# Optimization experiments

Hardware: AMD Instinct MI355X
Metric: run time of the kernel (lower is better)

## Reference

```python
import jax, jax.numpy as jnp
import numpy as np

N_HEAD, D_K = 8, 16

def _ln(x, g, b):
    m = jnp.mean(x, -1, keepdims=True)
    v = jnp.var(x, -1, keepdims=True)
    return (x - m) * jax.lax.rsqrt(v + 1e-5) * g + b

def _enc_layer(x, wq, bq, wk, bk, wv, bv, wo, bo, g1, be1, cw1, cb1, cw2, cb2, g2, be2):
    B, L, D = x.shape
    q = (x @ wq + bq).reshape(B, L, N_HEAD, D_K)
    k = (x @ wk + bk).reshape(B, L, N_HEAD, D_K)
    v = (x @ wv + bv).reshape(B, L, N_HEAD, D_K)
    attn = jnp.einsum('blhd,bmhd->bhlm', q, k) / jnp.sqrt(jnp.float32(D_K))
    attn = jax.nn.softmax(attn, axis=-1)
    o = jnp.einsum('bhlm,bmhd->blhd', attn, v).reshape(B, L, -1)
    x = _ln(o @ wo + bo + x, g1, be1)          # post-LN residual (MHA)
    h = jax.nn.relu(x @ cw1 + cb1)             # 1x1 conv == linear
    return _ln(h @ cw2 + cb2 + x, g2, be2)     # post-LN residual (FFN)

def setup_inputs() -> dict:
    key = jax.random.key(0)
    ks = jax.random.split(key, 20)
    N, D, NNZ = 100000, 128, 2000000
    B, L, NL, DI = 32, 256, 2, 512
    s = 0.02
    inp = {}
    inp['ego'] = jax.random.normal(ks[0], (N, D), jnp.float32)
    inp['vals'] = jax.random.uniform(ks[1], (NNZ,), jnp.float32) / 20.0  # ~normalized adj values
    inp['W1'] = jax.random.normal(ks[2], (D, D), jnp.float32) * s
    inp['b1'] = jnp.zeros((D,), jnp.float32)
    inp['W2'] = jax.random.normal(ks[3], (D, D), jnp.float32) * s
    inp['b2'] = jnp.zeros((D,), jnp.float32)
    inp['enc_in'] = jax.random.normal(ks[4], (B, L, D), jnp.float32)
    inp['wq'] = jax.random.normal(ks[5], (NL, D, D), jnp.float32) * s
    inp['bq'] = jnp.zeros((NL, D), jnp.float32)
    inp['wk'] = jax.random.normal(ks[6], (NL, D, D), jnp.float32) * s
    inp['bk'] = jnp.zeros((NL, D), jnp.float32)
    inp['wv'] = jax.random.normal(ks[7], (NL, D, D), jnp.float32) * s
    inp['bv'] = jnp.zeros((NL, D), jnp.float32)
    inp['wo'] = jax.random.normal(ks[8], (NL, D, D), jnp.float32) * s
    inp['bo'] = jnp.zeros((NL, D), jnp.float32)
    inp['ln1_g'] = jnp.ones((NL, D), jnp.float32)
    inp['ln1_b'] = jnp.zeros((NL, D), jnp.float32)
    inp['cw1'] = jax.random.normal(ks[9], (NL, D, DI), jnp.float32) * s
    inp['cb1'] = jnp.zeros((NL, DI), jnp.float32)
    inp['cw2'] = jax.random.normal(ks[10], (NL, DI, D), jnp.float32) * s
    inp['cb2'] = jnp.zeros((NL, D), jnp.float32)
    inp['ln2_g'] = jnp.ones((NL, D), jnp.float32)
    inp['ln2_b'] = jnp.zeros((NL, D), jnp.float32)
    inp['rows'] = jnp.sort(jax.random.randint(ks[11], (NNZ,), 0, N, jnp.int32))
    inp['cols'] = jax.random.randint(ks[12], (NNZ,), 0, N, jnp.int32)
    return inp

def reference(ego, vals, W1, b1, W2, b2, enc_in, wq, bq, wk, bk, wv, bv, wo, bo,
              ln1_g, ln1_b, cw1, cb1, cw2, cb2, ln2_g, ln2_b, rows, cols):
    N = ego.shape[0]
    # sparse A_in @ ego  (COO SpMM via gather + segment_sum)
    side = jax.ops.segment_sum(vals[:, None] * ego[cols], rows, num_segments=N)
    # bi-interaction aggregator (dropout=identity in eval)
    sum_emb = jax.nn.leaky_relu((ego + side) @ W1 + b1)
    bi_emb = jax.nn.leaky_relu((ego * side) @ W2 + b2)
    agg = sum_emb + bi_emb
    # transformer encoder over edge sequences
    x = enc_in
    for i in range(wq.shape[0]):
        x = _enc_layer(x, wq[i], bq[i], wk[i], bk[i], wv[i], bv[i], wo[i], bo[i],
                       ln1_g[i], ln1_b[i], cw1[i], cb1[i], cw2[i], cb2[i], ln2_g[i], ln2_b[i])
    return (agg, x)
```

## Files before the change

### kernel.cpp

```cpp
#include <hip/hip_runtime.h>

typedef __attribute__((ext_vector_type(8))) short bf16x8;
typedef __attribute__((ext_vector_type(4))) float f32x4;

__device__ __forceinline__ unsigned short f2b(float f) {
    union { float f; unsigned int i; } u; u.f = f;
    return (unsigned short)((u.i + 0x7FFFu + ((u.i >> 16) & 1u)) >> 16);
}
__device__ __forceinline__ unsigned int packbf2(float a, float b) {
    return (unsigned int)f2b(a) | ((unsigned int)f2b(b) << 16);
}

__device__ __forceinline__ void spmm_block(
    const unsigned int* __restrict__ egob, const float* __restrict__ vals,
    const int* __restrict__ rows, const int* __restrict__ cols,
    float* __restrict__ side, int nnz, int blk)
{
    int tid = threadIdx.x;
    int wave = tid >> 6, lane = tid & 63;
    int e0 = blk * 256 + wave * 64;
    if (e0 >= nnz) return;

    int idx = e0 + lane;
    int last = nnz - 1;
    bool ok = idx < nnz;
    int safe = ok ? idx : last;
    int my_row = rows[safe];
    int my_col = cols[safe];
    float my_val = ok ? vals[safe] : 0.f;

    unsigned int pre[16];
    #pragma unroll
    for (int j = 0; j < 16; ++j) {
        unsigned int c = (unsigned int)__builtin_amdgcn_readlane(my_col, j);
        pre[j] = *(egob + ((size_t)c << 6) + lane);
    }

    float ax = 0.f, ay = 0.f;
    int cur = __builtin_amdgcn_readlane(my_row, 0);
    #pragma unroll
    for (int e = 0; e < 64; ++e) {
        int r = __builtin_amdgcn_readlane(my_row, e);
        float vv = __int_as_float(__builtin_amdgcn_readlane(__float_as_int(my_val), e));
        unsigned int u = pre[e & 15];
        if (e < 48) {
            unsigned int c = (unsigned int)__builtin_amdgcn_readlane(my_col, e + 16);
            pre[e & 15] = *(egob + ((size_t)c << 6) + lane);
        }
        if (r != cur) {
            atomicAdd(&side[(size_t)cur * 128 + lane * 2], ax);
            atomicAdd(&side[(size_t)cur * 128 + lane * 2 + 1], ay);
            ax = 0.f; ay = 0.f; cur = r;
        }
        ax = fmaf(vv, __uint_as_float(u << 16), ax);
        ay = fmaf(vv, __uint_as_float(u & 0xFFFF0000u), ay);
    }
    atomicAdd(&side[(size_t)cur * 128 + lane * 2], ax);
    atomicAdd(&side[(size_t)cur * 128 + lane * 2 + 1], ay);
}

#define LDAB 40
#define LDBI2 136
#define LDKV 16

__device__ __forceinline__ void gemm2_core(
    const float* __restrict__ A, const float* __restrict__ W,
    const float* __restrict__ bias, const float* __restrict__ R,
    const float* __restrict__ g, const float* __restrict__ bta,
    float* __restrict__ C, int M, int N, int K, int act,
    int bm, int bn, unsigned short* As, unsigned short* Bs,
    float* redS, float* redSS)
{
    int tid = threadIdx.x, wave = tid >> 6, lane = tid & 63;
    int lm = lane & 15, quad = lane >> 4;
    int wm = wave >> 1, wn = wave & 1;

    f32x4 acc[2][4];
    #pragma unroll
    for (int i = 0; i < 2; ++i)
        #pragma unroll
        for (int j = 0; j < 4; ++j) acc[i][j] = (f32x4)(0.f);

    for (int k0 = 0; k0 < K; k0 += 32) {
        {
            int m = tid >> 2, kc = (tid & 3) * 8;
            const float* p = A + (size_t)(bm + m) * K + k0 + kc;
            float4 a0 = *(const float4*)p, a1 = *(const float4*)(p + 4);
            uint4 pk;
            pk.x = packbf2(a0.x, a0.y); pk.y = packbf2(a0.z, a0.w);
            pk.z = packbf2(a1.x, a1.y); pk.w = packbf2(a1.z, a1.w);
            *(uint4*)&As[m * LDAB + kc] = pk;
        }
        {
            int nn = tid & 127, kh = (tid >> 7) * 16;
            const float* p = W + (size_t)(k0 + kh) * N + bn + nn;
            float w[16];
            #pragma unroll
            for (int j = 0; j < 16; ++j) w[j] = p[(size_t)j * N];
            uint4 pk;
            pk.x = packbf2(w[0], w[1]);  pk.y = packbf2(w[2], w[3]);
            pk.z = packbf2(w[4], w[5]);  pk.w = packbf2(w[6], w[7]);
            *(uint4*)&Bs[nn * LDAB + kh] = pk;
            pk.x = packbf2(w[8], w[9]);  pk.y = packbf2(w[10], w[11]);
            pk.z = packbf2(w[12], w[13]); pk.w = packbf2(w[14], w[15]);
            *(uint4*)&Bs[nn * LDAB + kh + 8] = pk;
        }
        __syncthreads();
        bf16x8 af[2], bfr[4];
        #pragma unroll
        for (int mi = 0; mi < 2; ++mi)
            af[mi] = *(bf16x8*)&As[(wm * 32 + mi * 16 + lm) * LDAB + quad * 8];
        #pragma unroll
        for (int ni = 0; ni < 4; ++ni)
            bfr[ni] = *(bf16x8*)&Bs[(wn * 64 + ni * 16 + lm) * LDAB + quad * 8];
        #pragma unroll
        for (int mi = 0; mi < 2; ++mi)
            #pragma unroll
            for (int ni = 0; ni < 4; ++ni)
                acc[mi][ni] = __builtin_amdgcn_mfma_f32_16x16x32_bf16(
                    af[mi], bfr[ni], acc[mi][ni], 0, 0, 0);
        __syncthreads();
    }

    #pragma unroll
    for (int mi = 0; mi < 2; ++mi) {
        #pragma unroll
        for (int r = 0; r < 4; ++r) {
            int row = bm + wm * 32 + mi * 16 + quad * 4 + r;
            #pragma unroll
            for (int ni = 0; ni < 4; ++ni) {
                int col = bn + wn * 64 + ni * 16 + lm;
                float v = acc[mi][ni][r] + bias[col];
                if (R) v += R[(size_t)row * N + col];
                if (act) v = fmaxf(v, 0.f);
                acc[mi][ni][r] = v;
            }
        }
    }

    if (g) {
        #pragma unroll
        for (int mi = 0; mi < 2; ++mi) {
            #pragma unroll
            for (int r = 0; r < 4; ++r) {
                float s = 0.f, ss = 0.f;
                #pragma unroll
                for (int ni = 0; ni < 4; ++ni) {
                    float v = acc[mi][ni][r];
                    s += v; ss = fmaf(v, v, ss);
                }
                #pragma unroll
                for (int off = 1; off < 16; off <<= 1) {
                    s  += __shfl_xor(s, off, 64);
                    ss += __shfl_xor(ss, off, 64);
                }
                if (lm == 0) {
                    int lr = wm * 32 + mi * 16 + quad * 4 + r;
                    redS[wn * 64 + lr] = s;
                    redSS[wn * 64 + lr] = ss;
                }
            }
        }
        __syncthreads();
        #pragma unroll
        for (int mi = 0; mi < 2; ++mi) {
            #pragma unroll
            for (int r = 0; r < 4; ++r) {
                int lr = wm * 32 + mi * 16 + quad * 4 + r;
                int row = bm + lr;
                float s = redS[lr] + redS[64 + lr];
                float ss = redSS[lr] + redSS[64 + lr];
                float mean = s * (1.f / 128.f);
                float var = ss * (1.f / 128.f) - mean * mean;
                float rstd = rsqrtf(var + 1e-5f);
                #pragma unroll
                for (int ni = 0; ni < 4; ++ni) {
                    int col = wn * 64 + ni * 16 + lm;
                    float y = (acc[mi][ni][r] - mean) * rstd * g[col] + bta[col];
                    C[(size_t)row * 128 + col] = y;
                }
            }
        }
    } else {
        #pragma unroll
        for (int mi = 0; mi < 2; ++mi) {
            #pragma unroll
            for (int r = 0; r < 4; ++r) {
                int row = bm + wm * 32 + mi * 16 + quad * 4 + r;
                #pragma unroll
                for (int ni = 0; ni < 4; ++ni) {
                    int col = bn + wn * 64 + ni * 16 + lm;
                    C[(size_t)row * N + col] = acc[mi][ni][r];
                }
            }
        }
    }
}

__device__ __forceinline__ void bi_core4(
    const float* __restrict__ ego, const float* __restrict__ side,
    const unsigned short* __restrict__ W1t, const unsigned short* __restrict__ W2t,
    const float* __restrict__ b1, const float* __restrict__ b2,
    float* __restrict__ out, int M, int bm,
    unsigned short* Us, unsigned short* Ms)
{
    int tid = threadIdx.x, wave = tid >> 6, lane = tid & 63;
    int lm = lane & 15, quad = lane >> 4;
    int wm = wave >> 1, wn = wave & 1;

    f32x4 acc1[2][4], acc2[2][4];
    #pragma unroll
    for (int i = 0; i < 2; ++i)
        #pragma unroll
        for (int j = 0; j < 4; ++j) { acc1[i][j] = (f32x4)(0.f); acc2[i][j] = (f32x4)(0.f); }

    {
        int m = tid >> 2, kc = (tid & 3) * 32;
        int gm = bm + m;
        float e[32], s[32];
        if (gm < M) {
            const float* pe = ego + (size_t)gm * 128 + kc;
            const float* ps = side + (size_t)gm * 128 + kc;
            #pragma unroll
            for (int j = 0; j < 8; ++j) {
                float4 ev = *(const float4*)(pe + j * 4);
                float4 sv = *(const float4*)(ps + j * 4);
                e[j*4+0] = ev.x; e[j*4+1] = ev.y; e[j*4+2] = ev.z; e[j*4+3] = ev.w;
                s[j*4+0] = sv.x; s[j*4+1] = sv.y; s[j*4+2] = sv.z; s[j*4+3] = sv.w;
            }
        } else {
            #pragma unroll
            for (int j = 0; j < 32; ++j) { e[j] = 0.f; s[j] = 0.f; }
        }
        #pragma unroll
        for (int j = 0; j < 4; ++j) {
            int b0 = j * 8;
            uint4 pu, pv;
            pu.x = packbf2(e[b0+0]+s[b0+0], e[b0+1]+s[b0+1]);
            pu.y = packbf2(e[b0+2]+s[b0+2], e[b0+3]+s[b0+3]);
            pu.z = packbf2(e[b0+4]+s[b0+4], e[b0+5]+s[b0+5]);
            pu.w = packbf2(e[b0+6]+s[b0+6], e[b0+7]+s[b0+7]);
            pv.x = packbf2(e[b0+0]*s[b0+0], e[b0+1]*s[b0+1]);
            pv.y = packbf2(e[b0+2]*s[b0+2], e[b0+3]*s[b0+3]);
            pv.z = packbf2(e[b0+4]*s[b0+4], e[b0+5]*s[b0+5]);
            pv.w = packbf2(e[b0+6]*s[b0+6], e[b0+7]*s[b0+7]);
            *(uint4*)&Us[m * LDBI2 + kc + b0] = pu;
            *(uint4*)&Ms[m * LDBI2 + kc + b0] = pv;
        }
    }
    __syncthreads();

    #pragma unroll
    for (int ks = 0; ks < 4; ++ks) {
        bf16x8 au[2], am[2], bf1[4], bf2[4];
        #pragma unroll
        for (int mi = 0; mi < 2; ++mi) {
            int off = (wm * 32 + mi * 16 + lm) * LDBI2 + ks * 32 + quad * 8;
            au[mi] = *(bf16x8*)&Us[off];
            am[mi] = *(bf16x8*)&Ms[off];
        }
        #pragma unroll
        for (int ni = 0; ni < 4; ++ni) {
            size_t n = (size_t)(wn * 64 + ni * 16 + lm);
            size_t koff = n * 128 + ks * 32 + quad * 8;
            bf1[ni] = *(const bf16x8*)(W1t + koff);
            bf2[ni] = *(const bf16x8*)(W2t + koff);
        }
        #pragma unroll
        for (int mi = 0; mi < 2; ++mi)
            #pragma unroll
            for (int ni = 0; ni < 4; ++ni) {
                acc1[mi][ni] = __builtin_amdgcn_mfma_f32_16x16x32_bf16(
                    au[mi], bf1[ni], acc1[mi][ni], 0, 0, 0);
                acc2[mi][ni] = __builtin_amdgcn_mfma_f32_16x16x32_bf16(
                    am[mi], bf2[ni], acc2[mi][ni], 0, 0, 0);
            }
    }
    #pragma unroll
    for (int mi = 0; mi < 2; ++mi) {
        #pragma unroll
        for (int r = 0; r < 4; ++r) {
            int row = bm + wm * 32 + mi * 16 + quad * 4 + r;
            if (row < M) {
                #pragma unroll
                for (int ni = 0; ni < 4; ++ni) {
                    int col = wn * 64 + ni * 16 + lm;
                    float v1 = acc1[mi][ni][r] + b1[col];
                    v1 = v1 > 0.f ? v1 : 0.01f * v1;
                    float v2 = acc2[mi][ni][r] + b2[col];
                    v2 = v2 > 0.f ? v2 : 0.01f * v2;
                    out[(size_t)row * 128 + col] = v1 + v2;
                }
            }
        }
    }
}

__device__ __forceinline__ void attn_block(
    const float* __restrict__ q, const float* __restrict__ k,
    const float* __restrict__ v, float* __restrict__ o, int NH,
    int blk, float* Ks, float* Vs)
{
    const int L = 256, DK = 16;
    int bh = blk >> 2, qq = blk & 3;
    int b = bh / NH, h = bh % NH;
    int tid = threadIdx.x;
    int qi = tid >> 2, seg = tid & 3;

    int lq = qq * 64 + qi;
    size_t qbase = ((size_t)(b * L + lq) * NH + h) * DK;
    float qr[16];
    #pragma unroll
    for (int d4 = 0; d4 < 4; ++d4) {
        float4 t = *(const float4*)(q + qbase + d4 * 4);
        qr[d4*4+0] = t.x * 0.25f; qr[d4*4+1] = t.y * 0.25f;
        qr[d4*4+2] = t.z * 0.25f; qr[d4*4+3] = t.w * 0.25f;
    }
    float acc[16];
    #pragma unroll
    for (int d = 0; d < 16; ++d) acc[d] = 0.f;
    float mmax = -1e30f, ssum = 0.f;

    for (int c0 = 0; c0 < L; c0 += 128) {
        __syncthreads();
        for (int i = tid; i < 128 * 4; i += 256) {
            int ll = i >> 2, d4 = (i & 3) * 4;
            size_t gg = ((size_t)(b * L + c0 + ll) * NH + h) * DK + d4;
            *(float4*)&Ks[ll * LDKV + d4] = *(const float4*)(k + gg);
            *(float4*)&Vs[ll * LDKV + d4] = *(const float4*)(v + gg);
        }
        __syncthreads();

        for (int i = 0; i < 32; ++i) {
            int kk = (i << 2) | seg;
            const float* kr = &Ks[kk * LDKV];
            float dot = 0.f;
            #pragma unroll
            for (int d4 = 0; d4 < 4; ++d4) {
                float4 kv = *(const float4*)&kr[d4 * 4];
                dot = fmaf(qr[d4*4+0], kv.x, dot);
                dot = fmaf(qr[d4*4+1], kv.y, dot);
                dot = fmaf(qr[d4*4+2], kv.z, dot);
                dot = fmaf(qr[d4*4+3], kv.w, dot);
            }
            if (dot > mmax) {
                float alpha = __expf(mmax - dot);
                ssum *= alpha;
                #pragma unroll
                for (int d = 0; d < 16; ++d) acc[d] *= alpha;
                mmax = dot;
            }
            float p = __expf(dot - mmax);
            ssum += p;
            const float* vr = &Vs[kk * LDKV];
            #pragma unroll
            for (int d4 = 0; d4 < 4; ++d4) {
                float4 vv = *(const float4*)&vr[d4 * 4];
                acc[d4*4+0] = fmaf(p, vv.x, acc[d4*4+0]);
                acc[d4*4+1] = fmaf(p, vv.y, acc[d4*4+1]);
                acc[d4*4+2] = fmaf(p, vv.z, acc[d4*4+2]);
                acc[d4*4+3] = fmaf(p, vv.w, acc[d4*4+3]);
            }
        }
    }

    float m1 = fmaxf(mmax, __shfl_xor(mmax, 1, 64));
    float m2 = fmaxf(m1, __shfl_xor(m1, 2, 64));
    float f = __expf(mmax - m2);
    float sl = ssum * f;
    sl += __shfl_xor(sl, 1, 64);
    sl += __shfl_xor(sl, 2, 64);
    #pragma unroll
    for (int d = 0; d < 16; ++d) {
        float a = acc[d] * f;
        a += __shfl_xor(a, 1, 64);
        a += __shfl_xor(a, 2, 64);
        acc[d] = a;
    }
    if (seg == 0) {
        float inv = 1.f / sl;
        #pragma unroll
        for (int d4 = 0; d4 < 4; ++d4) {
            float4 t;
            t.x = acc[d4*4+0] * inv; t.y = acc[d4*4+1] * inv;
            t.z = acc[d4*4+2] * inv; t.w = acc[d4*4+3] * inv;
            *(float4*)(o + qbase + d4 * 4) = t;
        }
    }
}


__global__ __launch_bounds__(256) void qkv2_pre(
    const float* __restrict__ A,
    const float* __restrict__ wq, const float* __restrict__ wk, const float* __restrict__ wv,
    const float* __restrict__ bq, const float* __restrict__ bk, const float* __restrict__ bv,
    float* __restrict__ Q, float* __restrict__ Ko, float* __restrict__ V, int M, int encGy,
    float* __restrict__ side, int Nn,
    const float* __restrict__ ego, unsigned int* __restrict__ egob,
    const float* __restrict__ W1, const float* __restrict__ W2,
    unsigned short* __restrict__ W1t, unsigned short* __restrict__ W2t,
    int encN, int ZB, int CB, int WTB)
{
    __shared__ unsigned short As[64 * LDAB];
    __shared__ unsigned short Bs[128 * LDAB];
    __shared__ float redS[128], redSS[128];
    int gid = blockIdx.x;
    int tid = threadIdx.x;
    if (gid >= encN) {
        int j = gid - encN;
        if (j < ZB) {
            size_t n4 = (size_t)Nn * 32;
            float4 z = make_float4(0.f, 0.f, 0.f, 0.f);
            for (size_t i = (size_t)j * 256 + tid; i < n4; i += (size_t)ZB * 256)
                ((float4*)side)[i] = z;
        } else if (j < ZB + CB) {
            int c = j - ZB;
            size_t n4 = (size_t)Nn * 32;
            for (size_t i = (size_t)c * 256 + tid; i < n4; i += (size_t)CB * 256) {
                float4 a = *(const float4*)(ego + i * 4);
                uint2 p;
                p.x = packbf2(a.x, a.y);
                p.y = packbf2(a.z, a.w);
                *(uint2*)(egob + i * 2) = p;
            }
        } else {
            int c = j - ZB - CB;
            for (int ch = c * 256 + tid; ch < 4096; ch += WTB * 256) {
                int w = ch >> 11, rem = ch & 2047;
                int n = rem >> 4, k8 = rem & 15;
                const float* src = w ? W2 : W1;
                unsigned short* dst = w ? W2t : W1t;
                float t[8];
                #pragma unroll
                for (int jj = 0; jj < 8; ++jj)
                    t[jj] = src[(size_t)(k8 * 8 + jj) * 128 + n];
                uint4 pk;
                pk.x = packbf2(t[0], t[1]); pk.y = packbf2(t[2], t[3]);
                pk.z = packbf2(t[4], t[5]); pk.w = packbf2(t[6], t[7]);
                *(uint4*)&dst[(size_t)n * 128 + k8 * 8] = pk;
            }
        }
        return;
    }
    int sel = gid / encGy, by = gid % encGy;
    const float* W = (sel == 0) ? wq : (sel == 1) ? wk : wv;
    const float* b = (sel == 0) ? bq : (sel == 1) ? bk : bv;
    float* C = (sel == 0) ? Q : (sel == 1) ? Ko : V;
    gemm2_core(A, W, b, nullptr, nullptr, nullptr, C, M, 128, 128, 0,
               by * 64, 0, As, Bs, redS, redSS);
}

__global__ __launch_bounds__(256) void qkv2_spmm(
    const float* __restrict__ A,
    const float* __restrict__ wq, const float* __restrict__ wk, const float* __restrict__ wv,
    const float* __restrict__ bq, const float* __restrict__ bk, const float* __restrict__ bv,
    float* __restrict__ Q, float* __restrict__ Ko, float* __restrict__ V, int M, int encGy,
    const unsigned int* __restrict__ egob, const float* __restrict__ vals,
    const int* __restrict__ rows, const int* __restrict__ cols,
    float* __restrict__ side, int nnz, int spmmBase, int encN)
{
    __shared__ unsigned short As[64 * LDAB];
    __shared__ unsigned short Bs[128 * LDAB];
    __shared__ float redS[128], redSS[128];
    int gid = blockIdx.x;
    if (gid >= encN) {
        spmm_block(egob, vals, rows, cols, side, nnz, spmmBase + gid - encN);
        return;
    }
    int sel = gid / encGy, by = gid % encGy;
    const float* W = (sel == 0) ? wq : (sel == 1) ? wk : wv;
    const float* b = (sel == 0) ? bq : (sel == 1) ? bk : bv;
    float* C = (sel == 0) ? Q : (sel == 1) ? Ko : V;
    gemm2_core(A, W, b, nullptr, nullptr, nullptr, C, M, 128, 128, 0,
               by * 64, 0, As, Bs, redS, redSS);
}

__global__ __launch_bounds__(256) void gemm2_spmm(
    const float* __restrict__ A, const float* __restrict__ W,
    const float* __restrict__ bias, const float* __restrict__ R,
    const float* __restrict__ g, const float* __restrict__ bta,
    float* __restrict__ C, int M, int N, int K, int act, int encGy,
    const unsigned int* __restrict__ egob, const float* __restrict__ vals,
    const int* __restrict__ rows, const int* __restrict__ cols,
    float* __restrict__ side, int nnz, int spmmBase, int encN)
{
    __shared__ unsigned short As[64 * LDAB];
    __shared__ unsigned short Bs[128 * LDAB];
    __shared__ float redS[128], redSS[128];
    int gid = blockIdx.x;
    if (gid >= encN) {
        spmm_block(egob, vals, rows, cols, side, nnz, spmmBase + gid - encN);
        return;
    }
    int bx = gid / encGy, by = gid % encGy;
    gemm2_core(A, W, bias, R, g, bta, C, M, N, K, act,
               by * 64, bx * 128, As, Bs, redS, redSS);
}

__global__ __launch_bounds__(256) void gemm2_bi4(
    const float* __restrict__ A, const float* __restrict__ W,
    const float* __restrict__ bias, const float* __restrict__ R,
    const float* __restrict__ g, const float* __restrict__ bta,
    float* __restrict__ C, int M, int N, int K, int act, int encGy,
    const float* __restrict__ ego, const float* __restrict__ side,
    const unsigned short* __restrict__ W1t, const unsigned short* __restrict__ W2t,
    const float* __restrict__ b1, const float* __restrict__ b2,
    float* __restrict__ out, int Mbi, int biBase, int biCnt)
{
    __shared__ uint4 smem4[34816 / 16];
    char* smem = (char*)smem4;
    int gid = blockIdx.x;
    if (gid < biCnt) {
        int bb = biBase + gid;
        unsigned short* Us = (unsigned short*)smem;
        unsigned short* Ms = (unsigned short*)(smem + 17408);
        bi_core4(ego, side, W1t, W2t, b1, b2, out, Mbi, bb * 64, Us, Ms);
    } else {
        int egid = gid - biCnt;
        unsigned short* As = (unsigned short*)smem;
        unsigned short* Bs = (unsigned short*)(smem + 5120);
        float* redS  = (float*)(smem + 15360);
        float* redSS = (float*)(smem + 15360 + 512);
        int bx = egid / encGy, by = egid % encGy;
        gemm2_core(A, W, bias, R, g, bta, C, M, N, K, act,
                   by * 64, bx * 128, As, Bs, redS, redSS);
    }
}

__global__ __launch_bounds__(256) void attn_spmm(
    const float* __restrict__ q, const float* __restrict__ k,
    const float* __restrict__ v, float* __restrict__ o, int NH,
    const unsigned int* __restrict__ egob, const float* __restrict__ vals,
    const int* __restrict__ rows, const int* __restrict__ cols,
    float* __restrict__ side, int nnz, int spmmBase, int encN)
{
    __shared__ float Ks[128 * LDKV];
    __shared__ float Vs[128 * LDKV];
    int gid = blockIdx.x;
    if (gid >= encN) {
        spmm_block(egob, vals, rows, cols, side, nnz, spmmBase + gid - encN);
        return;
    }
    attn_block(q, k, v, o, NH, gid, Ks, Vs);
}

extern "C" void kernel_launch(void* const* d_in, const int* in_sizes, int n_in,
                              void* d_out, int out_size, void* d_ws, size_t ws_size,
                              hipStream_t stream) {
    const float* ego    = (const float*)d_in[0];
    const float* vals   = (const float*)d_in[1];
    const float* W1     = (const float*)d_in[2];
    const float* b1     = (const float*)d_in[3];
    const float* W2     = (const float*)d_in[4];
    const float* b2     = (const float*)d_in[5];
    const float* enc_in = (const float*)d_in[6];
    const float* wq  = (const float*)d_in[7];
    const float* bq  = (const float*)d_in[8];
    const float* wk  = (const float*)d_in[9];
    const float* bk  = (const float*)d_in[10];
    const float* wv  = (const float*)d_in[11];
    const float* bv  = (const float*)d_in[12];
    const float* wo  = (const float*)d_in[13];
    const float* bo  = (const float*)d_in[14];
    const float* ln1_g = (const float*)d_in[15];
    const float* ln1_b = (const float*)d_in[16];
    const float* cw1 = (const float*)d_in[17];
    const float* cb1 = (const float*)d_in[18];
    const float* cw2 = (const float*)d_in[19];
    const float* cb2 = (const float*)d_in[20];
    const float* ln2_g = (const float*)d_in[21];
    const float* ln2_b = (const float*)d_in[22];
    const int* rows = (const int*)d_in[23];
    const int* cols = (const int*)d_in[24];

    const int D = 128, DI = 512, NH = 8, L = 256;
    const int Nn   = in_sizes[0] / D;
    const int nnz  = in_sizes[1];
    const int NL   = in_sizes[7] / (D * D);
    const int Menc = in_sizes[6] / D;
    const int Bb   = Menc / L;

    float* ws = (float*)d_ws;
    size_t off = 0;
    float* side = ws + off; off += (size_t)Nn * D;
    float* Qb = ws + off; off += (size_t)Menc * D;
    float* Kb = ws + off; off += (size_t)Menc * D;
    float* Vb = ws + off; off += (size_t)Menc * D;
    float* Ob = ws + off; off += (size_t)Menc * D;
    float* XA = ws + off; off += (size_t)Menc * D;
    float* XB = ws + off; off += (size_t)Menc * D;
    float* Hb = ws + off; off += (size_t)Menc * DI;
    unsigned int* egob = (unsigned int*)(ws + off); off += (size_t)Nn * (D / 2);
    unsigned short* W1t = (unsigned short*)(ws + off); off += (size_t)D * D / 2;
    unsigned short* W2t = (unsigned short*)(ws + off); off += (size_t)D * D / 2;

    float* outAgg = (float*)d_out;
    float* outX   = (float*)d_out + (size_t)Nn * D;

    const int spmmBlocks = (nnz + 255) / 256;
    const int nSpmmStages = 5 * NL - 3;
    const int perS = (spmmBlocks + nSpmmStages - 1) / nSpmmStages;
    const int biTiles = (Nn + 63) / 64;
    const int perB = (biTiles + 1) / 2;
    const int biStart = 5 * NL - 1;
    const int encGy = Menc / 64;
    const int ZB = 512, CB = 1024, WTB = 16;
    int sidx = 0, sci = 0, bci = 0;

    const float* x = enc_in;
    for (int i = 0; i < NL; ++i) {
        const size_t wOff = (size_t)i * D * D;
        int base, cnt;
        #define SPMM_CHUNK base = sci * perS; cnt = spmmBlocks - base; \
                           if (cnt < 0) cnt = 0; if (cnt > perS) cnt = perS; sci++
        #define BI_CHUNK   base = bci * perB; cnt = biTiles - base; \
                           if (cnt < 0) cnt = 0; if (cnt > perB) cnt = perB; bci++

        sidx++;
        if (sidx == 1) {
            qkv2_pre<<<3 * encGy + ZB + CB + WTB, 256, 0, stream>>>(
                x, wq + wOff, wk + wOff, wv + wOff,
                bq + (size_t)i * D, bk + (size_t)i * D, bv + (size_t)i * D,
                Qb, Kb, Vb, Menc, encGy,
                side, Nn, ego, egob, W1, W2, W1t, W2t, 3 * encGy, ZB, CB, WTB);
        } else {
            SPMM_CHUNK;
            qkv2_spmm<<<3 * encGy + cnt, 256, 0, stream>>>(
                x, wq + wOff, wk + wOff, wv + wOff,
                bq + (size_t)i * D, bk + (size_t)i * D, bv + (size_t)i * D,
                Qb, Kb, Vb, Menc, encGy,
                egob, vals, rows, cols, side, nnz, base, 3 * encGy);
        }

        sidx++;
        SPMM_CHUNK;
        attn_spmm<<<Bb * NH * 4 + cnt, 256, 0, stream>>>(
            Qb, Kb, Vb, Ob, NH,
            egob, vals, rows, cols, side, nnz, base, Bb * NH * 4);

        sidx++;
        SPMM_CHUNK;
        gemm2_spmm<<<encGy + cnt, 256, 0, stream>>>(
            Ob, wo + wOff, bo + (size_t)i * D, x,
            ln1_g + (size_t)i * D, ln1_b + (size_t)i * D, XA, Menc, D, D, 0, encGy,
            egob, vals, rows, cols, side, nnz, base, encGy);

        sidx++;
        if (sidx >= biStart) {
            BI_CHUNK;
            gemm2_bi4<<<4 * encGy + cnt, 256, 0, stream>>>(
                XA, cw1 + (size_t)i * D * DI, cb1 + (size_t)i * DI, nullptr,
                nullptr, nullptr, Hb, Menc, DI, D, 1, encGy,
                ego, side, W1t, W2t, b1, b2, outAgg, Nn, base, cnt);
        } else {
            SPMM_CHUNK;
            gemm2_spmm<<<4 * encGy + cnt, 256, 0, stream>>>(
                XA, cw1 + (size_t)i * D * DI, cb1 + (size_t)i * DI, nullptr,
                nullptr, nullptr, Hb, Menc, DI, D, 1, encGy,
                egob, vals, rows, cols, side, nnz, base, 4 * encGy);
        }

        sidx++;
        float* dst = (i == NL - 1) ? outX : XB;
        if (sidx >= biStart) {
            BI_CHUNK;
            gemm2_bi4<<<encGy + cnt, 256, 0, stream>>>(
                Hb, cw2 + (size_t)i * DI * D, cb2 + (size_t)i * D, XA,
                ln2_g + (size_t)i * D, ln2_b + (size_t)i * D, dst, Menc, D, DI, 0, encGy,
                ego, side, W1t, W2t, b1, b2, outAgg, Nn, base, cnt);
        } else {
            SPMM_CHUNK;
            gemm2_spmm<<<encGy + cnt, 256, 0, stream>>>(
                Hb, cw2 + (size_t)i * DI * D, cb2 + (size_t)i * D, XA,
                ln2_g + (size_t)i * D, ln2_b + (size_t)i * D, dst, Menc, D, DI, 0, encGy,
                egob, vals, rows, cols, side, nnz, base, encGy);
        }
        #undef SPMM_CHUNK
        #undef BI_CHUNK
        x = XB;
    }
}
```

Before: 463.4 us.

## Pre-transpose encoder weights to bf16 once and read B fragments from global

The first kernel launch now also converts every encoder layer's wq/wk/wv/wo/cw1/cw2 weights into transposed bf16 layouts in a workspace buffer. A new GEMM core loads B fragments straight from that buffer instead of staging fp32 weights through shared memory on every tile. It also stages 128-wide K chunks of A, which cuts shared memory use and the number of barriers. The trade-offs are extra work in the prologue kernel, more global loads of weight fragments per wave, and a change to the LDS layout. The old gemm2_core is left in place with its LayerNorm path removed.

Result: no change. 466.3 us (+0.6%).

```diff
diff --git a/kernel.cpp b/kernel.cpp
--- a/kernel.cpp
+++ b/kernel.cpp
@@ -123,7 +123,82 @@
     }
 
     #pragma unroll
-    for (int mi = 0; mi < 2; ++mi) {
+    for (int mi = 0; mi < 2; ++mi)
+        #pragma unroll
+        for (int r = 0; r < 4; ++r) {
+            int row = bm + wm * 32 + mi * 16 + quad * 4 + r;
+            #pragma unroll
+            for (int ni = 0; ni < 4; ++ni) {
+                int col = bn + wn * 64 + ni * 16 + lm;
+                float v = acc[mi][ni][r] + bias[col];
+                if (R) v += R[(size_t)row * N + col];
+                if (act) v = fmaxf(v, 0.f);
+                C[(size_t)row * N + col] = v;
+            }
+        }
+    (void)g; (void)bta; (void)redS; (void)redSS;
+}
+
+__device__ __forceinline__ void gemm3_core(
+    const float* __restrict__ A, const unsigned short* __restrict__ Wt,
+    const float* __restrict__ bias, const float* __restrict__ R,
+    const float* __restrict__ g, const float* __restrict__ bta,
+    float* __restrict__ C, int M, int N, int K, int act,
+    int bm, int bn, unsigned short* As, float* redS, float* redSS)
+{
+    int tid = threadIdx.x, wave = tid >> 6, lane = tid & 63;
+    int lm = lane & 15, quad = lane >> 4;
+    int wm = wave >> 1, wn = wave & 1;
+
+    f32x4 acc[2][4];
+    #pragma unroll
+    for (int i = 0; i < 2; ++i)
+        #pragma unroll
+        for (int j = 0; j < 4; ++j) acc[i][j] = (f32x4)(0.f);
+
+    for (int kch = 0; kch < K; kch += 128) {
+        if (kch) __syncthreads();
+        {
+            int m = tid >> 2, kc = (tid & 3) * 32;
+            const float* p = A + (size_t)(bm + m) * K + kch + kc;
+            float a[32];
+            #pragma unroll
+            for (int j = 0; j < 8; ++j) {
+                float4 av = *(const float4*)(p + j * 4);
+                a[j*4+0] = av.x; a[j*4+1] = av.y; a[j*4+2] = av.z; a[j*4+3] = av.w;
+            }
+            #pragma unroll
+            for (int j = 0; j < 4; ++j) {
+                int b0 = j * 8;
+                uint4 pk;
+                pk.x = packbf2(a[b0+0], a[b0+1]); pk.y = packbf2(a[b0+2], a[b0+3]);
+                pk.z = packbf2(a[b0+4], a[b0+5]); pk.w = packbf2(a[b0+6], a[b0+7]);
+                *(uint4*)&As[m * LDBI2 + kc + b0] = pk;
+            }
+        }
+        __syncthreads();
+        #pragma unroll
+        for (int ks = 0; ks < 4; ++ks) {
+            bf16x8 af[2], bfr[4];
+            #pragma unroll
+            for (int mi = 0; mi < 2; ++mi)
+                af[mi] = *(bf16x8*)&As[(wm * 32 + mi * 16 + lm) * LDBI2 + ks * 32 + quad * 8];
+            #pragma unroll
+            for (int ni = 0; ni < 4; ++ni) {
+                size_t n = (size_t)(bn + wn * 64 + ni * 16 + lm);
+                bfr[ni] = *(const bf16x8*)(Wt + n * K + kch + ks * 32 + quad * 8);
+            }
+            #pragma unroll
+            for (int mi = 0; mi < 2; ++mi)
+                #pragma unroll
+                for (int ni = 0; ni < 4; ++ni)
+                    acc[mi][ni] = __builtin_amdgcn_mfma_f32_16x16x32_bf16(
+                        af[mi], bfr[ni], acc[mi][ni], 0, 0, 0);
+        }
+    }
+
+    #pragma unroll
+    for (int mi = 0; mi < 2; ++mi)
         #pragma unroll
         for (int r = 0; r < 4; ++r) {
             int row = bm + wm * 32 + mi * 16 + quad * 4 + r;
@@ -136,11 +211,10 @@
                 acc[mi][ni][r] = v;
             }
         }
-    }
 
     if (g) {
         #pragma unroll
-        for (int mi = 0; mi < 2; ++mi) {
+        for (int mi = 0; mi < 2; ++mi)
             #pragma unroll
             for (int r = 0; r < 4; ++r) {
                 float s = 0.f, ss = 0.f;
@@ -160,10 +234,9 @@
                     redSS[wn * 64 + lr] = ss;
                 }
             }
-        }
         __syncthreads();
         #pragma unroll
-        for (int mi = 0; mi < 2; ++mi) {
+        for (int mi = 0; mi < 2; ++mi)
             #pragma unroll
             for (int r = 0; r < 4; ++r) {
                 int lr = wm * 32 + mi * 16 + quad * 4 + r;
@@ -180,10 +253,9 @@
                     C[(size_t)row * 128 + col] = y;
                 }
             }
-        }
     } else {
         #pragma unroll
-        for (int mi = 0; mi < 2; ++mi) {
+        for (int mi = 0; mi < 2; ++mi)
             #pragma unroll
             for (int r = 0; r < 4; ++r) {
                 int row = bm + wm * 32 + mi * 16 + quad * 4 + r;
@@ -193,7 +265,6 @@
                     C[(size_t)row * N + col] = acc[mi][ni][r];
                 }
             }
-        }
     }
 }
 
@@ -277,7 +348,7 @@
             }
     }
     #pragma unroll
-    for (int mi = 0; mi < 2; ++mi) {
+    for (int mi = 0; mi < 2; ++mi)
         #pragma unroll
         for (int r = 0; r < 4; ++r) {
             int row = bm + wm * 32 + mi * 16 + quad * 4 + r;
@@ -293,7 +364,6 @@
                 }
             }
         }
-    }
 }
 
 __device__ __forceinline__ void attn_block(
@@ -399,7 +469,10 @@
     const float* __restrict__ ego, unsigned int* __restrict__ egob,
     const float* __restrict__ W1, const float* __restrict__ W2,
     unsigned short* __restrict__ W1t, unsigned short* __restrict__ W2t,
-    int encN, int ZB, int CB, int WTB)
+    const float* __restrict__ cw1, const float* __restrict__ cw2,
+    const float* __restrict__ wo,
+    unsigned short* __restrict__ wt, int NL,
+    int encN, int ZB, int CB, int WTB, int EWB)
 {
     __shared__ unsigned short As[64 * LDAB];
     __shared__ unsigned short Bs[128 * LDAB];
@@ -423,7 +496,7 @@
                 p.y = packbf2(a.z, a.w);
                 *(uint2*)(egob + i * 2) = p;
             }
-        } else {
+        } else if (j < ZB + CB + WTB) {
             int c = j - ZB - CB;
             for (int ch = c * 256 + tid; ch < 4096; ch += WTB * 256) {
                 int w = ch >> 11, rem = ch & 2047;
@@ -439,6 +512,38 @@
                 pk.z = packbf2(t[4], t[5]); pk.w = packbf2(t[6], t[7]);
                 *(uint4*)&dst[(size_t)n * 128 + k8 * 8] = pk;
             }
+        } else {
+            int c = j - ZB - CB - WTB;
+            int total = NL * 24576;
+            for (int u = c * 256 + tid; u < total; u += EWB * 256) {
+                int layer = u / 24576, w = u % 24576;
+                const float* src; unsigned short* dst; int K, N, n, k8;
+                if (w < 8192) {
+                    int mi = w >> 11, r = w & 2047;
+                    src = (mi == 0 ? wq : mi == 1 ? wk : mi == 2 ? wv : wo)
+                          + (size_t)layer * 16384;
+                    dst = wt + (size_t)layer * 196608 + mi * 16384;
+                    K = 128; N = 128; n = r >> 4; k8 = r & 15;
+                } else if (w < 16384) {
+                    int r = w - 8192;
+                    src = cw1 + (size_t)layer * 65536;
+                    dst = wt + (size_t)layer * 196608 + 65536;
+                    K = 128; N = 512; n = r >> 4; k8 = r & 15;
+                } else {
+                    int r = w - 16384;
+                    src = cw2 + (size_t)layer * 65536;
+                    dst = wt + (size_t)layer * 196608 + 131072;
+                    K = 512; N = 128; n = r >> 6; k8 = r & 63;
+                }
+                float t[8];
+                #pragma unroll
+                for (int jj = 0; jj < 8; ++jj)
+                    t[jj] = src[(size_t)(k8 * 8 + jj) * N + n];
+                uint4 pk;
+                pk.x = packbf2(t[0], t[1]); pk.y = packbf2(t[2], t[3]);
+                pk.z = packbf2(t[4], t[5]); pk.w = packbf2(t[6], t[7]);
+                *(uint4*)&dst[(size_t)n * K + k8 * 8] = pk;
+            }
         }
         return;
     }
@@ -450,17 +555,15 @@
                by * 64, 0, As, Bs, redS, redSS);
 }
 
-__global__ __launch_bounds__(256) void qkv2_spmm(
-    const float* __restrict__ A,
-    const float* __restrict__ wq, const float* __restrict__ wk, const float* __restrict__ wv,
+__global__ __launch_bounds__(256) void qkv3_spmm(
+    const float* __restrict__ A, const unsigned short* __restrict__ wtL,
     const float* __restrict__ bq, const float* __restrict__ bk, const float* __restrict__ bv,
     float* __restrict__ Q, float* __restrict__ Ko, float* __restrict__ V, int M, int encGy,
     const unsigned int* __restrict__ egob, const float* __restrict__ vals,
     const int* __restrict__ rows, const int* __restrict__ cols,
     float* __restrict__ side, int nnz, int spmmBase, int encN)
 {
-    __shared__ unsigned short As[64 * LDAB];
-    __shared__ unsigned short Bs[128 * LDAB];
+    __shared__ unsigned short As[64 * LDBI2];
     __shared__ float redS[128], redSS[128];
     int gid = blockIdx.x;
     if (gid >= encN) {
@@ -468,15 +571,15 @@
         return;
     }
     int sel = gid / encGy, by = gid % encGy;
-    const float* W = (sel == 0) ? wq : (sel == 1) ? wk : wv;
+    const unsigned short* Wt = wtL + sel * 16384;
     const float* b = (sel == 0) ? bq : (sel == 1) ? bk : bv;
     float* C = (sel == 0) ? Q : (sel == 1) ? Ko : V;
-    gemm2_core(A, W, b, nullptr, nullptr, nullptr, C, M, 128, 128, 0,
-               by * 64, 0, As, Bs, redS, redSS);
-}
-
-__global__ __launch_bounds__(256) void gemm2_spmm(
-    const float* __restrict__ A, const float* __restrict__ W,
+    gemm3_core(A, Wt, b, nullptr, nullptr, nullptr, C, M, 128, 128, 0,
+               by * 64, 0, As, redS, redSS);
+}
+
+__global__ __launch_bounds__(256) void gemm3_spmm(
+    const float* __restrict__ A, const unsigned short* __restrict__ Wt,
     const float* __restrict__ bias, const float* __restrict__ R,
     const float* __restrict__ g, const float* __restrict__ bta,
     float* __restrict__ C, int M, int N, int K, int act, int encGy,
@@ -484,8 +587,7 @@
     const int* __restrict__ rows, const int* __restrict__ cols,
     float* __restrict__ side, int nnz, int spmmBase, int encN)
 {
-    __shared__ unsigned short As[64 * LDAB];
-    __shared__ unsigned short Bs[128 * LDAB];
+    __shared__ unsigned short As[64 * LDBI2];
     __shared__ float redS[128], redSS[128];
     int gid = blockIdx.x;
     if (gid >= encN) {
@@ -493,12 +595,12 @@
         return;
     }
     int bx = gid / encGy, by = gid % encGy;
-    gemm2_core(A, W, bias, R, g, bta, C, M, N, K, act,
-               by * 64, bx * 128, As, Bs, redS, redSS);
-}
-
-__global__ __launch_bounds__(256) void gemm2_bi4(
-    const float* __restrict__ A, const float* __restrict__ W,
+    gemm3_core(A, Wt, bias, R, g, bta, C, M, N, K, act,
+               by * 64, bx * 128, As, redS, redSS);
+}
+
+__global__ __launch_bounds__(256) void gemm3_bi4(
+    const float* __restrict__ A, const unsigned short* __restrict__ Wt,
     const float* __restrict__ bias, const float* __restrict__ R,
     const float* __restrict__ g, const float* __restrict__ bta,
     float* __restrict__ C, int M, int N, int K, int act, int encGy,
@@ -518,12 +620,11 @@
     } else {
         int egid = gid - biCnt;
         unsigned short* As = (unsigned short*)smem;
-        unsigned short* Bs = (unsigned short*)(smem + 5120);
-        float* redS  = (float*)(smem + 15360);
-        float* redSS = (float*)(smem + 15360 + 512);
+        float* redS  = (float*)(smem + 17408);
+        float* redSS = (float*)(smem + 17408 + 512);
         int bx = egid / encGy, by = egid % encGy;
-        gemm2_core(A, W, bias, R, g, bta, C, M, N, K, act,
-                   by * 64, bx * 128, As, Bs, redS, redSS);
+        gemm3_core(A, Wt, bias, R, g, bta, C, M, N, K, act,
+                   by * 64, bx * 128, As, redS, redSS);
     }
 }
 
@@ -593,6 +694,7 @@
     unsigned int* egob = (unsigned int*)(ws + off); off += (size_t)Nn * (D / 2);
     unsigned short* W1t = (unsigned short*)(ws + off); off += (size_t)D * D / 2;
     unsigned short* W2t = (unsigned short*)(ws + off); off += (size_t)D * D / 2;
+    unsigned short* wt  = (unsigned short*)(ws + off); off += (size_t)NL * 196608 / 2;
 
     float* outAgg = (float*)d_out;
     float* outX   = (float*)d_out + (size_t)Nn * D;
@@ -604,12 +706,13 @@
     const int perB = (biTiles + 1) / 2;
     const int biStart = 5 * NL - 1;
     const int encGy = Menc / 64;
-    const int ZB = 512, CB = 1024, WTB = 16;
+    const int ZB = 512, CB = 1024, WTB = 16, EWB = 64;
     int sidx = 0, sci = 0, bci = 0;
 
     const float* x = enc_in;
     for (int i = 0; i < NL; ++i) {
         const size_t wOff = (size_t)i * D * D;
+        const unsigned short* wtL = wt + (size_t)i * 196608;
         int base, cnt;
         #define SPMM_CHUNK base = sci * perS; cnt = spmmBlocks - base; \
                            if (cnt < 0) cnt = 0; if (cnt > perS) cnt = perS; sci++
@@ -618,15 +721,16 @@
 
         sidx++;
         if (sidx == 1) {
-            qkv2_pre<<<3 * encGy + ZB + CB + WTB, 256, 0, stream>>>(
+            qkv2_pre<<<3 * encGy + ZB + CB + WTB + EWB, 256, 0, stream>>>(
                 x, wq + wOff, wk + wOff, wv + wOff,
                 bq + (size_t)i * D, bk + (size_t)i * D, bv + (size_t)i * D,
                 Qb, Kb, Vb, Menc, encGy,
-                side, Nn, ego, egob, W1, W2, W1t, W2t, 3 * encGy, ZB, CB, WTB);
+                side, Nn, ego, egob, W1, W2, W1t, W2t,
+                cw1, cw2, wo, wt, NL, 3 * encGy, ZB, CB, WTB, EWB);
         } else {
             SPMM_CHUNK;
-            qkv2_spmm<<<3 * encGy + cnt, 256, 0, stream>>>(
-                x, wq + wOff, wk + wOff, wv + wOff,
+            qkv3_spmm<<<3 * encGy + cnt, 256, 0, stream>>>(
+                x, wtL,
                 bq + (size_t)i * D, bk + (size_t)i * D, bv + (size_t)i * D,
                 Qb, Kb, Vb, Menc, encGy,
                 egob, vals, rows, cols, side, nnz, base, 3 * encGy);
@@ -640,22 +744,22 @@
 
         sidx++;
         SPMM_CHUNK;
-        gemm2_spmm<<<encGy + cnt, 256, 0, stream>>>(
-            Ob, wo + wOff, bo + (size_t)i * D, x,
+        gemm3_spmm<<<encGy + cnt, 256, 0, stream>>>(
+            Ob, wtL + 49152, bo + (size_t)i * D, x,
             ln1_g + (size_t)i * D, ln1_b + (size_t)i * D, XA, Menc, D, D, 0, encGy,
             egob, vals, rows, cols, side, nnz, base, encGy);
 
         sidx++;
         if (sidx >= biStart) {
             BI_CHUNK;
-            gemm2_bi4<<<4 * encGy + cnt, 256, 0, stream>>>(
-                XA, cw1 + (size_t)i * D * DI, cb1 + (size_t)i * DI, nullptr,
+            gemm3_bi4<<<4 * encGy + cnt, 256, 0, stream>>>(
+                XA, wtL + 65536, cb1 + (size_t)i * DI, nullptr,
                 nullptr, nullptr, Hb, Menc, DI, D, 1, encGy,
                 ego, side, W1t, W2t, b1, b2, outAgg, Nn, base, cnt);
         } else {
             SPMM_CHUNK;
-            gemm2_spmm<<<4 * encGy + cnt, 256, 0, stream>>>(
-                XA, cw1 + (size_t)i * D * DI, cb1 + (size_t)i * DI, nullptr,
+            gemm3_spmm<<<4 * encGy + cnt, 256, 0, stream>>>(
+                XA, wtL + 65536, cb1 + (size_t)i * DI, nullptr,
                 nullptr, nullptr, Hb, Menc, DI, D, 1, encGy,
                 egob, vals, rows, cols, side, nnz, base, 4 * encGy);
         }
@@ -664,14 +768,14 @@
         float* dst = (i == NL - 1) ? outX : XB;
         if (sidx >= biStart) {
             BI_CHUNK;
-            gemm2_bi4<<<encGy + cnt, 256, 0, stream>>>(
-                Hb, cw2 + (size_t)i * DI * D, cb2 + (size_t)i * D, XA,
+            gemm3_bi4<<<encGy + cnt, 256, 0, stream>>>(
+                Hb, wtL + 131072, cb2 + (size_t)i * D, XA,
                 ln2_g + (size_t)i * D, ln2_b + (size_t)i * D, dst, Menc, D, DI, 0, encGy,
                 ego, side, W1t, W2t, b1, b2, outAgg, Nn, base, cnt);
         } else {
             SPMM_CHUNK;
-            gemm2_spmm<<<encGy + cnt, 256, 0, stream>>>(
-                Hb, cw2 + (size_t)i * DI * D, cb2 + (size_t)i * D, XA,
+            gemm3_spmm<<<encGy + cnt, 256, 0, stream>>>(
+                Hb, wtL + 131072, cb2 + (size_t)i * D, XA,
                 ln2_g + (size_t)i * D, ln2_b + (size_t)i * D, dst, Menc, D, DI, 0, encGy,
                 egob, vals, rows, cols, side, nnz, base, encGy);
         }
```
